# Kernel optimization log

Hardware: AMD Instinct MI355X
Metric: run time of the kernel (lower is better)

## Reference

```python
import jax, jax.numpy as jnp
import numpy as np

N_LAYERS = 3
D = 32          # in = hidden = out channels (hardcoded in module)
N = 100_000     # nodes
E = 3_200_000   # edges (avg degree 32)
EPS = 1e-5
SLOPE = 0.01    # LeakyReLU default negative slope


def setup_inputs() -> dict:
    key = jax.random.key(0)
    ks = jax.random.split(key, 12)
    x = jax.random.normal(ks[0], (N, D), jnp.float32)
    edge_index = jax.random.randint(ks[1], (2, E), 0, N)
    edge_attr = jax.random.normal(ks[2], (E, 1), jnp.float32)  # unused by the conv
    s = 1.0 / np.sqrt(D)  # torch Linear default init range
    W = lambda k: jax.random.uniform(k, (N_LAYERS, D, D), jnp.float32, -s, s)
    b = lambda k: jax.random.uniform(k, (N_LAYERS, D), jnp.float32, -s, s)
    return dict(
        patch_embs=x, edge_index=edge_index, edge_attr=edge_attr,
        Wk=W(ks[3]), bk=b(ks[4]),   # lin_key   (applied to x_i / target)
        Wq=W(ks[5]), bq=b(ks[6]),   # lin_query (applied to x_j / source)
        Wv=W(ks[7]), bv=b(ks[8]),   # lin_value (applied to x_j / source)
        Ws=W(ks[9]), bs=b(ks[10]),  # lin_skip  (applied to x_i)
        gamma=jnp.ones((N_LAYERS, D), jnp.float32),
        beta=jnp.zeros((N_LAYERS, D), jnp.float32),
    )


def _res_gated_conv(x, Wk, bk, Wq, bq, Wv, bv, Ws, bs, src, dst):
    # Project per-node first (cheap), gather per-edge after.
    k = x @ Wk.T + bk   # [N,D] key   of target
    q = x @ Wq.T + bq   # [N,D] query of source
    v = x @ Wv.T + bv   # [N,D] value of source
    eta = jax.nn.sigmoid(k[dst] + q[src])          # [E,D] gate
    agg = jax.ops.segment_sum(eta * v[src], dst, num_segments=x.shape[0])
    return agg + (x @ Ws.T + bs)


def _batchnorm(x, g, b):
    mu = x.mean(axis=0)
    var = x.var(axis=0)  # biased, as in torch BN training forward
    return (x - mu) * jax.lax.rsqrt(var + EPS) * g + b


def _leaky(z):
    return jnp.where(z >= 0, z, SLOPE * z)


def reference(patch_embs, edge_index, edge_attr, Wk, bk, Wq, bq, Wv, bv, Ws, bs, gamma, beta):
    src, dst = edge_index[0], edge_index[1]
    h = patch_embs
    h = _batchnorm(_leaky(_res_gated_conv(h, Wk[0], bk[0], Wq[0], bq[0], Wv[0], bv[0], Ws[0], bs[0], src, dst)) + h, gamma[0], beta[0])
    h = _batchnorm(_leaky(_res_gated_conv(h, Wk[1], bk[1], Wq[1], bq[1], Wv[1], bv[1], Ws[1], bs[1], src, dst)) + h, gamma[1], beta[1])
    h = _batchnorm(_res_gated_conv(h, Wk[2], bk[2], Wq[2], bq[2], Wv[2], bv[2], Ws[2], bs[2], src, dst) + h, gamma[2], beta[2])
    return h
```

## Files before the change

kernel.cpp:

```cpp
#include <hip/hip_runtime.h>

#define DCH 32
#define EPSV 1e-5f
#define SLOPE 0.01f
#define SSTRIDE 16
#define BSH 7
#define BSZ 128
#define NBMAX 1024
#define CHUNK 8192
#define CAP 6144
#define LOG2E 1.4426950408889634f

#if defined(__has_builtin)
#  if __has_builtin(__builtin_amdgcn_exp2f)
#    define EXP2F(x) __builtin_amdgcn_exp2f(x)
#  endif
#  if __has_builtin(__builtin_amdgcn_rcpf)
#    define RCPF(x) __builtin_amdgcn_rcpf(x)
#  endif
#endif
#ifndef EXP2F
#  define EXP2F(x) exp2f(x)
#endif
#ifndef RCPF
#  define RCPF(x) (1.0f / (x))
#endif

__device__ __forceinline__ unsigned short f2bf(float x) {
    unsigned u = __float_as_uint(x);
    unsigned r = (u + 0x7FFFu + ((u >> 16) & 1u)) >> 16;
    return (unsigned short)r;
}

__global__ __launch_bounds__(256) void k_bucket_hist(const int* __restrict__ dst,
                                                     int* __restrict__ bcnt, int E, int NB) {
    __shared__ int h[NBMAX];
    const int t = threadIdx.x;
    const int e0 = blockIdx.x * CHUNK;
    const int e1 = min(e0 + CHUNK, E);
    if (NB <= NBMAX) {
        for (int j = t; j < NB; j += 256) h[j] = 0;
        __syncthreads();
        for (int e = e0 + t; e < e1; e += 256) atomicAdd(&h[dst[e] >> BSH], 1);
        __syncthreads();
        for (int j = t; j < NB; j += 256) if (h[j]) atomicAdd(&bcnt[j], h[j]);
    } else {
        for (int e = e0 + t; e < e1; e += 256) atomicAdd(&bcnt[dst[e] >> BSH], 1);
    }
}

__global__ __launch_bounds__(1024) void k_scan(const int* __restrict__ deg, int* __restrict__ off, int N) {
    __shared__ int wsum[16];
    __shared__ int woff[16];
    __shared__ int ctot;
    __shared__ int carry;
    const int t = threadIdx.x;
    const int lane = t & 63;
    const int w = t >> 6;
    if (t == 0) carry = 0;
    __syncthreads();
    for (int base = 0; base < N; base += 1024) {
        const int i = base + t;
        const int v = (i < N) ? deg[i] : 0;
        int incl = v;
        #pragma unroll
        for (int d = 1; d < 64; d <<= 1) {
            int tmp = __shfl_up(incl, d);
            if (lane >= d) incl += tmp;
        }
        if (lane == 63) wsum[w] = incl;
        __syncthreads();
        if (t < 16) {
            const int a = wsum[t];
            int in = a;
            #pragma unroll
            for (int d = 1; d < 16; d <<= 1) {
                int tmp = __shfl_up(in, d);
                if (t >= d) in += tmp;
            }
            woff[t] = in - a;
            if (t == 15) ctot = in;
        }
        __syncthreads();
        if (i < N) off[i] = carry + woff[w] + incl - v;
        __syncthreads();
        if (t == 0) carry += ctot;
        __syncthreads();
    }
    if (t == 0) off[N] = carry;
}

__global__ __launch_bounds__(256) void k_bucket_scatter(const int* __restrict__ src, const int* __restrict__ dst,
                                                        const int* __restrict__ boff, int* __restrict__ cur,
                                                        unsigned int* __restrict__ pairs, int E, int NB) {
    const int t = threadIdx.x;
    const int e0 = blockIdx.x * CHUNK;
    const int e1 = min(e0 + CHUNK, E);
    if (NB <= NBMAX) {
        __shared__ int cnt[NBMAX];
        __shared__ int base[NBMAX];
        for (int j = t; j < NB; j += 256) { cnt[j] = 0; }
        __syncthreads();
        for (int e = e0 + t; e < e1; e += 256) atomicAdd(&cnt[dst[e] >> BSH], 1);
        __syncthreads();
        for (int j = t; j < NB; j += 256) {
            const int c = cnt[j];
            if (c) base[j] = atomicAdd(&cur[j], c);
            cnt[j] = 0;
        }
        __syncthreads();
        for (int e = e0 + t; e < e1; e += 256) {
            const int d = dst[e];
            const int bk = d >> BSH;
            const int r = atomicAdd(&cnt[bk], 1);
            pairs[boff[bk] + base[bk] + r] = ((unsigned)src[e] << BSH) | (unsigned)(d & (BSZ - 1));
        }
    } else {
        for (int e = e0 + t; e < e1; e += 256) {
            const int d = dst[e];
            const int bk = d >> BSH;
            const int r = atomicAdd(&cur[bk], 1);
            pairs[boff[bk] + r] = ((unsigned)src[e] << BSH) | (unsigned)(d & (BSZ - 1));
        }
    }
}

__global__ __launch_bounds__(256) void k_build_csr(const unsigned int* __restrict__ pairs,
                                                   const int* __restrict__ boff,
                                                   int* __restrict__ deg, int* __restrict__ off,
                                                   int* __restrict__ ssrc, int N) {
    __shared__ int cnt[BSZ];
    __shared__ int scn[BSZ];
    __shared__ int rnk[BSZ];
    __shared__ int stage[CAP];
    const int t = threadIdx.x;
    const int b = blockIdx.x;
    const int begin = boff[b], end = boff[b + 1];
    const int total = end - begin;
    if (t < BSZ) { cnt[t] = 0; rnk[t] = 0; }
    __syncthreads();
    for (int i = begin + t; i < end; i += 256) atomicAdd(&cnt[pairs[i] & (BSZ - 1)], 1);
    __syncthreads();
    if (t < BSZ) scn[t] = cnt[t];
    __syncthreads();
    #pragma unroll
    for (int s = 1; s < BSZ; s <<= 1) {
        int add = 0;
        if (t < BSZ && t >= s) add = scn[t - s];
        __syncthreads();
        if (t < BSZ) scn[t] += add;
        __syncthreads();
    }
    const int node0 = b << BSH;
    if (t < BSZ && node0 + t < N) {
        deg[node0 + t] = cnt[t];
        off[node0 + t] = begin + scn[t] - cnt[t];
    }
    if (total <= CAP) {
        for (int i = begin + t; i < end; i += 256) {
            const unsigned u = pairs[i];
            const int nl = u & (BSZ - 1);
            const int r = atomicAdd(&rnk[nl], 1);
            stage[scn[nl] - cnt[nl] + r] = (int)(u >> BSH);
        }
        __syncthreads();
        for (int i = t; i < total; i += 256) ssrc[begin + i] = stage[i];
    } else {
        for (int i = begin + t; i < end; i += 256) {
            const unsigned u = pairs[i];
            const int nl = u & (BSZ - 1);
            const int r = atomicAdd(&rnk[nl], 1);
            ssrc[begin + scn[nl] - cnt[nl] + r] = (int)(u >> BSH);
        }
    }
}

__global__ __launch_bounds__(256) void k_project(
    const float* __restrict__ xin,
    const float* __restrict__ statsPrev, const float* __restrict__ gPrev, const float* __restrict__ bPrev,
    const float* __restrict__ Wk, const float* __restrict__ bk,
    const float* __restrict__ Wq, const float* __restrict__ bq,
    const float* __restrict__ Wv, const float* __restrict__ bv,
    const float* __restrict__ Ws, const float* __restrict__ bs,
    float* __restrict__ kout, uint4* __restrict__ qvout,
    float* __restrict__ zout, float* __restrict__ statsCur,
    int N, int do_bn, float invN)
{
    __shared__ float wk[DCH][DCH + 1], wq[DCH][DCH + 1], wv[DCH][DCH + 1], wsk[DCH][DCH + 1];
    __shared__ float xs[8][DCH];
    __shared__ unsigned short qvs[8][64];
    const int t = threadIdx.x;
    if (blockIdx.x == 0) {
        for (int i = t; i < 2048; i += 256) statsCur[i] = 0.f;
    }
    for (int i = t; i < DCH * DCH; i += 256) {
        const int c = i >> 5, d = i & 31;
        wk[c][d] = Wk[i];
        wq[c][d] = Wq[i];
        wv[c][d] = Wv[i];
        wsk[c][d] = Ws[i];
    }
    const int li = t >> 5;
    const int c  = t & 31;
    const int node = blockIdx.x * 8 + li;
    if (node < N) {
        float xv = xin[node * DCH + c];
        if (do_bn) {
            const float mn = statsPrev[c * SSTRIDE] * invN;
            const float var = statsPrev[1024 + c * SSTRIDE] * invN - mn * mn;
            const float sc = rsqrtf(var + EPSV) * gPrev[c];
            xv = (xv - mn) * sc + bPrev[c];
        }
        xs[li][c] = xv;
    }
    __syncthreads();
    if (node < N) {
        float aK = 0.f, aQ = 0.f, aV = 0.f, aS = 0.f;
        #pragma unroll
        for (int d = 0; d < DCH; ++d) {
            const float xv = xs[li][d];
            aK += xv * wk[c][d];
            aQ += xv * wq[c][d];
            aV += xv * wv[c][d];
            aS += xv * wsk[c][d];
        }
        const int o = node * DCH + c;
        kout[o] = -LOG2E * (aK + bk[c]);
        zout[o] = aS + bs[c];
        const int g = c >> 2, j = c & 3;
        qvs[li][g * 8 + j]     = f2bf(-LOG2E * (aQ + bq[c]));
        qvs[li][g * 8 + 4 + j] = f2bf(aV + bv[c]);
    }
    __syncthreads();
    if (t < 64) {
        const int ln = t >> 3, g = t & 7;
        const int nd = blockIdx.x * 8 + ln;
        if (nd < N) qvout[nd * 8 + g] = ((const uint4*)qvs[ln])[g];
    }
}

__global__ __launch_bounds__(256) void k_edges_csr(
    const int* __restrict__ off, const int* __restrict__ deg, const int* __restrict__ ssrc,
    const float4* __restrict__ kn4, const uint4* __restrict__ qv4,
    const float4* __restrict__ zprev4,
    const float* __restrict__ statsPrev, const float* __restrict__ gPrev, const float* __restrict__ bPrev,
    float4* __restrict__ z4,
    float* __restrict__ statsCur, int N, int do_leaky, int do_bn, float invN)
{
    const int t = threadIdx.x;
    const int p = t & 7;
    const int lane = t & 63;
    const int w = t >> 6;
    float scv[4] = {1.f, 1.f, 1.f, 1.f}, shv[4] = {0.f, 0.f, 0.f, 0.f};
    if (do_bn) {
        #pragma unroll
        for (int j = 0; j < 4; ++j) {
            const int c = p * 4 + j;
            const float mn = statsPrev[c * SSTRIDE] * invN;
            const float var = statsPrev[1024 + c * SSTRIDE] * invN - mn * mn;
            const float rs = rsqrtf(var + EPSV) * gPrev[c];
            scv[j] = rs;
            shv[j] = bPrev[c] - mn * rs;
        }
    }
    float s0 = 0.f, s1 = 0.f, s2 = 0.f, s3 = 0.f;
    float r0 = 0.f, r1 = 0.f, r2 = 0.f, r3 = 0.f;
    const int n = blockIdx.x * 32 + (t >> 3);
    if (n < N) {
        const int idx = n * 8 + p;
        const float4 kn = kn4[idx];
        float ax = 0.f, ay = 0.f, az = 0.f, aw = 0.f;
        const int beg = off[n];
        const int end = beg + deg[n];
        for (int e = beg; e < end; ++e) {
            const int s = ssrc[e];
            const uint4 u = qv4[(size_t)s * 8 + p];
            const float q0 = __uint_as_float(u.x << 16);
            const float q1 = __uint_as_float(u.x & 0xffff0000u);
            const float q2 = __uint_as_float(u.y << 16);
            const float q3 = __uint_as_float(u.y & 0xffff0000u);
            const float v0 = __uint_as_float(u.z << 16);
            const float v1 = __uint_as_float(u.z & 0xffff0000u);
            const float v2 = __uint_as_float(u.w << 16);
            const float v3 = __uint_as_float(u.w & 0xffff0000u);
            ax = fmaf(v0, RCPF(1.f + EXP2F(kn.x + q0)), ax);
            ay = fmaf(v1, RCPF(1.f + EXP2F(kn.y + q1)), ay);
            az = fmaf(v2, RCPF(1.f + EXP2F(kn.z + q2)), az);
            aw = fmaf(v3, RCPF(1.f + EXP2F(kn.w + q3)), aw);
        }
        float4 z = z4[idx];
        z.x += ax; z.y += ay; z.z += az; z.w += aw;
        if (do_leaky) {
            z.x = z.x >= 0.f ? z.x : SLOPE * z.x;
            z.y = z.y >= 0.f ? z.y : SLOPE * z.y;
            z.z = z.z >= 0.f ? z.z : SLOPE * z.z;
            z.w = z.w >= 0.f ? z.w : SLOPE * z.w;
        }
        const float4 hz = zprev4[idx];
        z.x += hz.x * scv[0] + shv[0];
        z.y += hz.y * scv[1] + shv[1];
        z.z += hz.z * scv[2] + shv[2];
        z.w += hz.w * scv[3] + shv[3];
        z4[idx] = z;
        s0 = z.x; s1 = z.y; s2 = z.z; s3 = z.w;
        r0 = z.x * z.x; r1 = z.y * z.y; r2 = z.z * z.z; r3 = z.w * z.w;
    }
    #pragma unroll
    for (int d = 8; d < 64; d <<= 1) {
        s0 += __shfl_down(s0, d); s1 += __shfl_down(s1, d);
        s2 += __shfl_down(s2, d); s3 += __shfl_down(s3, d);
        r0 += __shfl_down(r0, d); r1 += __shfl_down(r1, d);
        r2 += __shfl_down(r2, d); r3 += __shfl_down(r3, d);
    }
    __shared__ float sm[4][DCH], sq[4][DCH];
    if (lane < 8) {
        sm[w][p * 4 + 0] = s0; sm[w][p * 4 + 1] = s1; sm[w][p * 4 + 2] = s2; sm[w][p * 4 + 3] = s3;
        sq[w][p * 4 + 0] = r0; sq[w][p * 4 + 1] = r1; sq[w][p * 4 + 2] = r2; sq[w][p * 4 + 3] = r3;
    }
    __syncthreads();
    if (t < DCH) {
        const float a = sm[0][t] + sm[1][t] + sm[2][t] + sm[3][t];
        const float b = sq[0][t] + sq[1][t] + sq[2][t] + sq[3][t];
        atomicAdd(&statsCur[t * SSTRIDE], a);
        atomicAdd(&statsCur[1024 + t * SSTRIDE], b);
    }
}

__global__ __launch_bounds__(256) void k_bn(
    const float* __restrict__ z, const float* __restrict__ stats,
    const float* __restrict__ gamma, const float* __restrict__ beta,
    float* __restrict__ out, int total, float invN)
{
    const int i = blockIdx.x * 256 + threadIdx.x;
    if (i >= total) return;
    const int c = i & 31;
    const float mean = stats[c * SSTRIDE] * invN;
    const float var  = stats[1024 + c * SSTRIDE] * invN - mean * mean;
    out[i] = (z[i] - mean) * rsqrtf(var + EPSV) * gamma[c] + beta[c];
}

extern "C" void kernel_launch(void* const* d_in, const int* in_sizes, int n_in,
                              void* d_out, int out_size, void* d_ws, size_t ws_size,
                              hipStream_t stream) {
    const float* x     = (const float*)d_in[0];
    const int*   ei    = (const int*)  d_in[1];
    const float* Wk    = (const float*)d_in[3];
    const float* bk    = (const float*)d_in[4];
    const float* Wq    = (const float*)d_in[5];
    const float* bq    = (const float*)d_in[6];
    const float* Wv    = (const float*)d_in[7];
    const float* bv    = (const float*)d_in[8];
    const float* Ws    = (const float*)d_in[9];
    const float* bs    = (const float*)d_in[10];
    const float* gamma = (const float*)d_in[11];
    const float* beta  = (const float*)d_in[12];

    const int N = in_sizes[0] / DCH;
    const int E = in_sizes[1] / 2;
    const int NB = (N + BSZ - 1) >> BSH;
    const int* src = ei;
    const int* dst = ei + E;

    float* ws     = (float*)d_ws;
    float* kbuf   = ws;
    unsigned short* qvbuf = (unsigned short*)(kbuf + (size_t)N * DCH);
    float* zA     = (float*)qvbuf + (size_t)N * DCH;
    float* zB     = zA + (size_t)N * DCH;
    float* statsA = zB + (size_t)N * DCH;
    float* statsB = statsA + 2048;
    int*   deg    = (int*)(statsB + 2048);
    int*   off    = deg + N;
    int*   bcnt   = off + N;
    int*   boff   = bcnt + NB;
    int*   cur    = boff + NB + 1;
    unsigned int* pairs = (unsigned int*)(cur + NB);
    int*   ssrc   = (int*)(pairs + E);

    const int total = N * DCH;
    const float invN = 1.f / (float)N;

    hipMemsetAsync(bcnt, 0, (size_t)NB * sizeof(int), stream);
    hipMemsetAsync(cur, 0, (size_t)NB * sizeof(int), stream);
    const int nchunk = (E + CHUNK - 1) / CHUNK;
    k_bucket_hist<<<nchunk, 256, 0, stream>>>(dst, bcnt, E, NB);
    k_scan<<<1, 1024, 0, stream>>>(bcnt, boff, NB);
    k_bucket_scatter<<<nchunk, 256, 0, stream>>>(src, dst, boff, cur, pairs, E, NB);
    k_build_csr<<<NB, 256, 0, stream>>>(pairs, boff, deg, off, ssrc, N);

    const float* zprev = x;
    const float* statsPrev = nullptr;
    for (int l = 0; l < 3; ++l) {
        const size_t wo = (size_t)l * DCH * DCH;
        const size_t bo = (size_t)l * DCH;
        float* zcur = (l & 1) ? zB : zA;
        float* statsCur = (l & 1) ? statsB : statsA;
        const float* gPrev = (l > 0) ? gamma + (size_t)(l - 1) * DCH : gamma;
        const float* bPrev = (l > 0) ? beta + (size_t)(l - 1) * DCH : beta;
        const int do_bn = (l > 0) ? 1 : 0;
        const float* sPrev = do_bn ? statsPrev : statsA;

        k_project<<<(N + 7) / 8, 256, 0, stream>>>(
            zprev, sPrev, gPrev, bPrev,
            Wk + wo, bk + bo, Wq + wo, bq + bo, Wv + wo, bv + bo, Ws + wo, bs + bo,
            kbuf, (uint4*)qvbuf, zcur, statsCur, N, do_bn, invN);
        k_edges_csr<<<(N + 31) / 32, 256, 0, stream>>>(
            off, deg, ssrc, (const float4*)kbuf, (const uint4*)qvbuf,
            (const float4*)zprev, sPrev, gPrev, bPrev,
            (float4*)zcur, statsCur, N, (l < 2) ? 1 : 0, do_bn, invN);

        statsPrev = statsCur;
        zprev = zcur;
    }
    k_bn<<<(total + 255) / 256, 256, 0, stream>>>(
        zA, statsA, gamma + 2 * DCH, beta + 2 * DCH, (float*)d_out, total, invN);
}
```

Before: 606.9 us.

## Drop per-node CSR build; aggregate edges per bucket with shared-memory atomics

Result: slower. 2.250 ms (+270.8%).

```diff
diff --git a/kernel.cpp b/kernel.cpp
--- a/kernel.cpp
+++ b/kernel.cpp
@@ -8,7 +8,8 @@
 #define BSZ 128
 #define NBMAX 1024
 #define CHUNK 8192
-#define CAP 6144
+#define ZPAD 36
+#define KPAD 36
 #define LOG2E 1.4426950408889634f
 
 #if defined(__has_builtin)
@@ -121,56 +122,6 @@
             const int bk = d >> BSH;
             const int r = atomicAdd(&cur[bk], 1);
             pairs[boff[bk] + r] = ((unsigned)src[e] << BSH) | (unsigned)(d & (BSZ - 1));
-        }
-    }
-}
-
-__global__ __launch_bounds__(256) void k_build_csr(const unsigned int* __restrict__ pairs,
-                                                   const int* __restrict__ boff,
-                                                   int* __restrict__ deg, int* __restrict__ off,
-                                                   int* __restrict__ ssrc, int N) {
-    __shared__ int cnt[BSZ];
-    __shared__ int scn[BSZ];
-    __shared__ int rnk[BSZ];
-    __shared__ int stage[CAP];
-    const int t = threadIdx.x;
-    const int b = blockIdx.x;
-    const int begin = boff[b], end = boff[b + 1];
-    const int total = end - begin;
-    if (t < BSZ) { cnt[t] = 0; rnk[t] = 0; }
-    __syncthreads();
-    for (int i = begin + t; i < end; i += 256) atomicAdd(&cnt[pairs[i] & (BSZ - 1)], 1);
-    __syncthreads();
-    if (t < BSZ) scn[t] = cnt[t];
-    __syncthreads();
-    #pragma unroll
-    for (int s = 1; s < BSZ; s <<= 1) {
-        int add = 0;
-        if (t < BSZ && t >= s) add = scn[t - s];
-        __syncthreads();
-        if (t < BSZ) scn[t] += add;
-        __syncthreads();
-    }
-    const int node0 = b << BSH;
-    if (t < BSZ && node0 + t < N) {
-        deg[node0 + t] = cnt[t];
-        off[node0 + t] = begin + scn[t] - cnt[t];
-    }
-    if (total <= CAP) {
-        for (int i = begin + t; i < end; i += 256) {
-            const unsigned u = pairs[i];
-            const int nl = u & (BSZ - 1);
-            const int r = atomicAdd(&rnk[nl], 1);
-            stage[scn[nl] - cnt[nl] + r] = (int)(u >> BSH);
-        }
-        __syncthreads();
-        for (int i = t; i < total; i += 256) ssrc[begin + i] = stage[i];
-    } else {
-        for (int i = begin + t; i < end; i += 256) {
-            const unsigned u = pairs[i];
-            const int nl = u & (BSZ - 1);
-            const int r = atomicAdd(&rnk[nl], 1);
-            ssrc[begin + scn[nl] - cnt[nl] + r] = (int)(u >> BSH);
         }
     }
 }
@@ -239,23 +190,79 @@
     }
 }
 
-__global__ __launch_bounds__(256) void k_edges_csr(
-    const int* __restrict__ off, const int* __restrict__ deg, const int* __restrict__ ssrc,
-    const float4* __restrict__ kn4, const uint4* __restrict__ qv4,
+#define EDGE_PROC(u, a)                                                      \
+    do {                                                                     \
+        const int dl = (int)((u) & (BSZ - 1));                               \
+        const float4 kk = *(const float4*)&ks[dl * KPAD + p4];               \
+        const float q0 = __uint_as_float((a).x << 16);                       \
+        const float q1 = __uint_as_float((a).x & 0xffff0000u);               \
+        const float q2 = __uint_as_float((a).y << 16);                       \
+        const float q3 = __uint_as_float((a).y & 0xffff0000u);               \
+        const float v0 = __uint_as_float((a).z << 16);                       \
+        const float v1 = __uint_as_float((a).z & 0xffff0000u);               \
+        const float v2 = __uint_as_float((a).w << 16);                       \
+        const float v3 = __uint_as_float((a).w & 0xffff0000u);               \
+        float* zp = &zs[dl * ZPAD + p4];                                     \
+        atomicAdd(zp + 0, v0 * RCPF(1.f + EXP2F(kk.x + q0)));                \
+        atomicAdd(zp + 1, v1 * RCPF(1.f + EXP2F(kk.y + q1)));                \
+        atomicAdd(zp + 2, v2 * RCPF(1.f + EXP2F(kk.z + q2)));                \
+        atomicAdd(zp + 3, v3 * RCPF(1.f + EXP2F(kk.w + q3)));                \
+    } while (0)
+
+__global__ __launch_bounds__(256) void k_edges_bucket(
+    const unsigned int* __restrict__ pairs, const int* __restrict__ boff,
+    const float* __restrict__ kn,
+    const uint4* __restrict__ qv4,
     const float4* __restrict__ zprev4,
     const float* __restrict__ statsPrev, const float* __restrict__ gPrev, const float* __restrict__ bPrev,
     float4* __restrict__ z4,
     float* __restrict__ statsCur, int N, int do_leaky, int do_bn, float invN)
 {
+    __shared__ float zs[BSZ * ZPAD];
+    __shared__ float ks[BSZ * KPAD];
+    __shared__ float sm[4][DCH], sq[4][DCH];
     const int t = threadIdx.x;
+    const int b = blockIdx.x;
+    const int node0 = b << BSH;
+    const int nvalid = min(BSZ, N - node0);
+
+    for (int i = t; i < BSZ * ZPAD; i += 256) zs[i] = 0.f;
+    for (int i = t; i < nvalid * DCH; i += 256)
+        ks[(i >> 5) * KPAD + (i & 31)] = kn[(size_t)node0 * DCH + i];
+    __syncthreads();
+
     const int p = t & 7;
-    const int lane = t & 63;
-    const int w = t >> 6;
+    const int p4 = p * 4;
+    const int g = t >> 3;
+    const int begin = boff[b], end = boff[b + 1];
+
+    int e = begin + g;
+    for (; e + 96 < end; e += 128) {
+        const unsigned u0 = pairs[e];
+        const unsigned u1 = pairs[e + 32];
+        const unsigned u2 = pairs[e + 64];
+        const unsigned u3 = pairs[e + 96];
+        const uint4 a0 = qv4[(size_t)(u0 >> BSH) * 8 + p];
+        const uint4 a1 = qv4[(size_t)(u1 >> BSH) * 8 + p];
+        const uint4 a2 = qv4[(size_t)(u2 >> BSH) * 8 + p];
+        const uint4 a3 = qv4[(size_t)(u3 >> BSH) * 8 + p];
+        EDGE_PROC(u0, a0);
+        EDGE_PROC(u1, a1);
+        EDGE_PROC(u2, a2);
+        EDGE_PROC(u3, a3);
+    }
+    for (; e < end; e += 32) {
+        const unsigned u = pairs[e];
+        const uint4 a = qv4[(size_t)(u >> BSH) * 8 + p];
+        EDGE_PROC(u, a);
+    }
+    __syncthreads();
+
     float scv[4] = {1.f, 1.f, 1.f, 1.f}, shv[4] = {0.f, 0.f, 0.f, 0.f};
     if (do_bn) {
         #pragma unroll
         for (int j = 0; j < 4; ++j) {
-            const int c = p * 4 + j;
+            const int c = p4 + j;
             const float mn = statsPrev[c * SSTRIDE] * invN;
             const float var = statsPrev[1024 + c * SSTRIDE] * invN - mn * mn;
             const float rs = rsqrtf(var + EPSV) * gPrev[c];
@@ -265,46 +272,29 @@
     }
     float s0 = 0.f, s1 = 0.f, s2 = 0.f, s3 = 0.f;
     float r0 = 0.f, r1 = 0.f, r2 = 0.f, r3 = 0.f;
-    const int n = blockIdx.x * 32 + (t >> 3);
-    if (n < N) {
-        const int idx = n * 8 + p;
-        const float4 kn = kn4[idx];
-        float ax = 0.f, ay = 0.f, az = 0.f, aw = 0.f;
-        const int beg = off[n];
-        const int end = beg + deg[n];
-        for (int e = beg; e < end; ++e) {
-            const int s = ssrc[e];
-            const uint4 u = qv4[(size_t)s * 8 + p];
-            const float q0 = __uint_as_float(u.x << 16);
-            const float q1 = __uint_as_float(u.x & 0xffff0000u);
-            const float q2 = __uint_as_float(u.y << 16);
-            const float q3 = __uint_as_float(u.y & 0xffff0000u);
-            const float v0 = __uint_as_float(u.z << 16);
-            const float v1 = __uint_as_float(u.z & 0xffff0000u);
-            const float v2 = __uint_as_float(u.w << 16);
-            const float v3 = __uint_as_float(u.w & 0xffff0000u);
-            ax = fmaf(v0, RCPF(1.f + EXP2F(kn.x + q0)), ax);
-            ay = fmaf(v1, RCPF(1.f + EXP2F(kn.y + q1)), ay);
-            az = fmaf(v2, RCPF(1.f + EXP2F(kn.z + q2)), az);
-            aw = fmaf(v3, RCPF(1.f + EXP2F(kn.w + q3)), aw);
-        }
-        float4 z = z4[idx];
-        z.x += ax; z.y += ay; z.z += az; z.w += aw;
+    for (int m = t; m < nvalid * 8; m += 256) {
+        const int n = m >> 3;
+        float4 z = *(const float4*)&zs[n * ZPAD + p4];
+        const size_t gi = (size_t)node0 * 8 + m;
+        const float4 zi = z4[gi];
+        z.x += zi.x; z.y += zi.y; z.z += zi.z; z.w += zi.w;
         if (do_leaky) {
             z.x = z.x >= 0.f ? z.x : SLOPE * z.x;
             z.y = z.y >= 0.f ? z.y : SLOPE * z.y;
             z.z = z.z >= 0.f ? z.z : SLOPE * z.z;
             z.w = z.w >= 0.f ? z.w : SLOPE * z.w;
         }
-        const float4 hz = zprev4[idx];
+        const float4 hz = zprev4[gi];
         z.x += hz.x * scv[0] + shv[0];
         z.y += hz.y * scv[1] + shv[1];
         z.z += hz.z * scv[2] + shv[2];
         z.w += hz.w * scv[3] + shv[3];
-        z4[idx] = z;
-        s0 = z.x; s1 = z.y; s2 = z.z; s3 = z.w;
-        r0 = z.x * z.x; r1 = z.y * z.y; r2 = z.z * z.z; r3 = z.w * z.w;
-    }
+        z4[gi] = z;
+        s0 += z.x; s1 += z.y; s2 += z.z; s3 += z.w;
+        r0 += z.x * z.x; r1 += z.y * z.y; r2 += z.z * z.z; r3 += z.w * z.w;
+    }
+    const int lane = t & 63;
+    const int w = t >> 6;
     #pragma unroll
     for (int d = 8; d < 64; d <<= 1) {
         s0 += __shfl_down(s0, d); s1 += __shfl_down(s1, d);
@@ -312,17 +302,16 @@
         r0 += __shfl_down(r0, d); r1 += __shfl_down(r1, d);
         r2 += __shfl_down(r2, d); r3 += __shfl_down(r3, d);
     }
-    __shared__ float sm[4][DCH], sq[4][DCH];
     if (lane < 8) {
-        sm[w][p * 4 + 0] = s0; sm[w][p * 4 + 1] = s1; sm[w][p * 4 + 2] = s2; sm[w][p * 4 + 3] = s3;
-        sq[w][p * 4 + 0] = r0; sq[w][p * 4 + 1] = r1; sq[w][p * 4 + 2] = r2; sq[w][p * 4 + 3] = r3;
+        sm[w][p4 + 0] = s0; sm[w][p4 + 1] = s1; sm[w][p4 + 2] = s2; sm[w][p4 + 3] = s3;
+        sq[w][p4 + 0] = r0; sq[w][p4 + 1] = r1; sq[w][p4 + 2] = r2; sq[w][p4 + 3] = r3;
     }
     __syncthreads();
     if (t < DCH) {
         const float a = sm[0][t] + sm[1][t] + sm[2][t] + sm[3][t];
-        const float b = sq[0][t] + sq[1][t] + sq[2][t] + sq[3][t];
+        const float bb = sq[0][t] + sq[1][t] + sq[2][t] + sq[3][t];
         atomicAdd(&statsCur[t * SSTRIDE], a);
-        atomicAdd(&statsCur[1024 + t * SSTRIDE], b);
+        atomicAdd(&statsCur[1024 + t * SSTRIDE], bb);
     }
 }
 
@@ -368,13 +357,10 @@
     float* zB     = zA + (size_t)N * DCH;
     float* statsA = zB + (size_t)N * DCH;
     float* statsB = statsA + 2048;
-    int*   deg    = (int*)(statsB + 2048);
-    int*   off    = deg + N;
-    int*   bcnt   = off + N;
+    int*   bcnt   = (int*)(statsB + 2048);
     int*   boff   = bcnt + NB;
     int*   cur    = boff + NB + 1;
     unsigned int* pairs = (unsigned int*)(cur + NB);
-    int*   ssrc   = (int*)(pairs + E);
 
     const int total = N * DCH;
     const float invN = 1.f / (float)N;
@@ -385,7 +371,6 @@
     k_bucket_hist<<<nchunk, 256, 0, stream>>>(dst, bcnt, E, NB);
     k_scan<<<1, 1024, 0, stream>>>(bcnt, boff, NB);
     k_bucket_scatter<<<nchunk, 256, 0, stream>>>(src, dst, boff, cur, pairs, E, NB);
-    k_build_csr<<<NB, 256, 0, stream>>>(pairs, boff, deg, off, ssrc, N);
 
     const float* zprev = x;
     const float* statsPrev = nullptr;
@@ -403,8 +388,8 @@
             zprev, sPrev, gPrev, bPrev,
             Wk + wo, bk + bo, Wq + wo, bq + bo, Wv + wo, bv + bo, Ws + wo, bs + bo,
             kbuf, (uint4*)qvbuf, zcur, statsCur, N, do_bn, invN);
-        k_edges_csr<<<(N + 31) / 32, 256, 0, stream>>>(
-            off, deg, ssrc, (const float4*)kbuf, (const uint4*)qvbuf,
+        k_edges_bucket<<<NB, 256, 0, stream>>>(
+            pairs, boff, kbuf, (const uint4*)qvbuf,
             (const float4*)zprev, sPrev, gPrev, bPrev,
             (float4*)zcur, statsCur, N, (l < 2) ? 1 : 0, do_bn, invN);
 
```
